# Kernel tuning notes

Hardware: AMD Instinct MI355X
Metric: run time of the kernel (lower is better)

The kernel has to match this reference:

```python
import jax, jax.numpy as jnp
import numpy as np

H = 64  # hidden_dim


def _gru_cell(x, h, W_ih, W_hh, b_ih, b_hh):
    # PyTorch GRU gate order: reset (r), update (z), new (n)
    gx = x @ W_ih.T + b_ih            # [B, 3H]
    gh = h @ W_hh.T + b_hh            # [B, 3H]
    xr, xz, xn = jnp.split(gx, 3, axis=-1)
    hr, hz, hn = jnp.split(gh, 3, axis=-1)
    r = jax.nn.sigmoid(xr + hr)
    z = jax.nn.sigmoid(xz + hz)
    n = jnp.tanh(xn + r * hn)
    return (1.0 - z) * n + z * h


def setup_inputs() -> dict:
    key = jax.random.key(0)
    ks = jax.random.split(key, 11)
    B, T, F_in, A = 1024, 512, 128, 18
    s = 0.05
    return {
        "state": jax.random.normal(ks[0], (B, T, F_in), dtype=jnp.float32),
        "W_ih_l0": jax.random.normal(ks[1], (3 * H, F_in), dtype=jnp.float32) * s,
        "W_hh_l0": jax.random.normal(ks[2], (3 * H, H), dtype=jnp.float32) * s,
        "b_ih_l0": jax.random.normal(ks[3], (3 * H,), dtype=jnp.float32) * s,
        "b_hh_l0": jax.random.normal(ks[4], (3 * H,), dtype=jnp.float32) * s,
        "W_ih_l1": jax.random.normal(ks[5], (3 * H, H), dtype=jnp.float32) * s,
        "W_hh_l1": jax.random.normal(ks[6], (3 * H, H), dtype=jnp.float32) * s,
        "b_ih_l1": jax.random.normal(ks[7], (3 * H,), dtype=jnp.float32) * s,
        "b_hh_l1": jax.random.normal(ks[8], (3 * H,), dtype=jnp.float32) * s,
        "fc3_w": jax.random.normal(ks[9], (A, H), dtype=jnp.float32) * s,
        "fc3_b": jax.random.normal(ks[10], (A,), dtype=jnp.float32) * s,
    }


def reference(state, W_ih_l0, W_hh_l0, b_ih_l0, b_hh_l0,
              W_ih_l1, W_hh_l1, b_ih_l1, b_hh_l1, fc3_w, fc3_b):
    B = state.shape[0]
    h0 = jnp.zeros((B, H), dtype=state.dtype)
    h1 = jnp.zeros((B, H), dtype=state.dtype)
    xs = jnp.swapaxes(state, 0, 1)  # [T, B, F]

    def step(carry, x_t):
        h0, h1 = carry
        h0 = _gru_cell(x_t, h0, W_ih_l0, W_hh_l0, b_ih_l0, b_hh_l0)
        h1 = _gru_cell(h0, h1, W_ih_l1, W_hh_l1, b_ih_l1, b_hh_l1)
        return (h0, h1), None

    (_, h1_last), _ = jax.lax.scan(step, (h0, h1), xs)
    # out[:, -1] of the top GRU layer == final h1; then relu -> linear
    actions = jax.nn.relu(h1_last) @ fc3_w.T + fc3_b
    return actions
```

## Files before the change

### kernel.cpp

```cpp
#include <hip/hip_runtime.h>


#define Tn 512
#define Fn 128
#define Hn 64
#define An 18
#define HS 72

typedef _Float16 half8 __attribute__((ext_vector_type(8)));
typedef float f32x4 __attribute__((ext_vector_type(4)));

#define MFMA(a, b, c) __builtin_amdgcn_mfma_f32_16x16x32_f16((a), (b), (c), 0, 0, 0)

static __device__ __forceinline__ float sigm(float x) {
    return __builtin_amdgcn_rcpf(1.0f + __builtin_amdgcn_exp2f(-1.4426950408889634f * x));
}
static __device__ __forceinline__ float tanh_f(float x) {
    return 2.0f * __builtin_amdgcn_rcpf(1.0f + __builtin_amdgcn_exp2f(-2.8853900817779268f * x)) - 1.0f;
}

__global__ __launch_bounds__(512) void gru_fused(
    const float* __restrict__ state,
    const float* __restrict__ Wih0, const float* __restrict__ Whh0,
    const float* __restrict__ bih0, const float* __restrict__ bhh0,
    const float* __restrict__ Wih1, const float* __restrict__ Whh1,
    const float* __restrict__ bih1, const float* __restrict__ bhh1,
    const float* __restrict__ fcw, const float* __restrict__ fcb,
    float* __restrict__ out)
{
    const int tid  = threadIdx.x;
    const int wv8  = tid >> 6;
    const int lane = tid & 63, c = lane & 15, q = lane >> 4;
    const int wv   = wv8 & 3;
    const int r0   = blockIdx.x * 16;
    const int gc   = wv * 16 + c;
    const int roleB = (wv8 >= 4);

    __shared__ __align__(16) _Float16 h0buf[2][16 * HS];
    __shared__ __align__(16) _Float16 h1buf[2][16 * HS];
    __shared__ float fbuf[16 * 64];

    for (int i = tid; i < 2 * 16 * HS; i += 512) {
        (&h0buf[0][0])[i] = (_Float16)0.0f;
        (&h1buf[0][0])[i] = (_Float16)0.0f;
    }

    half8 W[18];
    f32x4 bias0, bias1, bias2, bias3;
    f32x4 xf32[8];
    half8 xf[4];
    f32x4 hreg = {0.f, 0.f, 0.f, 0.f};
    const float* srow = state + (size_t)(r0 + c) * (Tn * Fn);

    if (!roleB) {
#pragma unroll
        for (int gsel = 0; gsel < 3; ++gsel) {
            const int g = gsel * 64 + gc;
#pragma unroll
            for (int ks = 0; ks < 4; ++ks) {
                const float* p = Wih0 + g * Fn + ks * 32 + q * 8;
#pragma unroll
                for (int j = 0; j < 8; ++j) W[gsel * 4 + ks][j] = (_Float16)p[j];
            }
#pragma unroll
            for (int ks = 0; ks < 2; ++ks) {
                const float* p = Whh0 + g * Hn + ks * 32 + q * 8;
#pragma unroll
                for (int j = 0; j < 8; ++j) W[12 + gsel * 2 + ks][j] = (_Float16)p[j];
            }
        }
        {
            const float b0 = bih0[gc] + bhh0[gc];
            const float b1 = bih0[64 + gc] + bhh0[64 + gc];
            const float b2 = bih0[128 + gc];
            const float b3 = bhh0[128 + gc];
            bias0 = (f32x4){b0, b0, b0, b0};
            bias1 = (f32x4){b1, b1, b1, b1};
            bias2 = (f32x4){b2, b2, b2, b2};
            bias3 = (f32x4){b3, b3, b3, b3};
        }
#pragma unroll
        for (int ks = 0; ks < 4; ++ks) {
            xf32[2 * ks]     = *(const f32x4*)(srow + ks * 32 + q * 8);
            xf32[2 * ks + 1] = *(const f32x4*)(srow + ks * 32 + q * 8 + 4);
        }
#pragma unroll
        for (int ks = 0; ks < 4; ++ks)
#pragma unroll
            for (int i = 0; i < 4; ++i) {
                xf[ks][i]     = (_Float16)xf32[2 * ks][i];
                xf[ks][4 + i] = (_Float16)xf32[2 * ks + 1][i];
            }
#pragma unroll
        for (int ks = 0; ks < 4; ++ks) {
            xf32[2 * ks]     = *(const f32x4*)(srow + Fn + ks * 32 + q * 8);
            xf32[2 * ks + 1] = *(const f32x4*)(srow + Fn + ks * 32 + q * 8 + 4);
        }
    } else {
#pragma unroll
        for (int gsel = 0; gsel < 3; ++gsel) {
            const int g = gsel * 64 + gc;
#pragma unroll
            for (int ks = 0; ks < 2; ++ks) {
                const float* pa = Wih1 + g * Hn + ks * 32 + q * 8;
                const float* pb = Whh1 + g * Hn + ks * 32 + q * 8;
#pragma unroll
                for (int j = 0; j < 8; ++j) {
                    W[gsel * 2 + ks][j]     = (_Float16)pa[j];
                    W[6 + gsel * 2 + ks][j] = (_Float16)pb[j];
                }
            }
        }
        const float br_ = bih1[gc] + bhh1[gc];
        const float bz_ = bih1[64 + gc] + bhh1[64 + gc];
        const float bxn = bih1[128 + gc];
        const float bhn = bhh1[128 + gc];
        bias0 = (f32x4){br_, br_, br_, br_};
        bias1 = (f32x4){bz_, bz_, bz_, bz_};
        bias2 = (f32x4){bxn, bxn, bxn, bxn};
        bias3 = (f32x4){bhn, bhn, bhn, bhn};
    }

    const int ardr = c * HS + q * 8;
    const int wrow = (q * 4) * HS + gc;
    const f32x4 z4 = {0.f, 0.f, 0.f, 0.f};

    for (int t = 0; t <= Tn; ++t) {
        __syncthreads();
        const int pr = (t & 1) ^ 1, pw = t & 1;
        if (!roleB) {
            if (t < Tn) {
                const half8 hf0 = *(const half8*)&h0buf[pr][ardr];
                const half8 hf1 = *(const half8*)&h0buf[pr][ardr + 32];
                __builtin_amdgcn_s_setprio(1);
                f32x4 ar = MFMA(xf[0], W[0], bias0);  ar = MFMA(xf[1], W[1], ar);
                f32x4 az = MFMA(xf[0], W[4], bias1);  az = MFMA(xf[1], W[5], az);
                f32x4 an = MFMA(xf[0], W[8], bias2);  an = MFMA(xf[1], W[9], an);
                f32x4 br = MFMA(xf[2], W[2], z4);     br = MFMA(xf[3], W[3], br);
                f32x4 bz = MFMA(xf[2], W[6], z4);     bz = MFMA(xf[3], W[7], bz);
                f32x4 bn = MFMA(xf[2], W[10], z4);    bn = MFMA(xf[3], W[11], bn);
                br = MFMA(hf0, W[12], br);  br = MFMA(hf1, W[13], br);
                bz = MFMA(hf0, W[14], bz);  bz = MFMA(hf1, W[15], bz);
                f32x4 hn = MFMA(hf0, W[16], bias3);  hn = MFMA(hf1, W[17], hn);
                __builtin_amdgcn_s_setprio(0);
                if (t < Tn - 1) {
#pragma unroll
                    for (int ks = 0; ks < 4; ++ks)
#pragma unroll
                        for (int i = 0; i < 4; ++i) {
                            xf[ks][i]     = (_Float16)xf32[2 * ks][i];
                            xf[ks][4 + i] = (_Float16)xf32[2 * ks + 1][i];
                        }
                    const int tnx = (t + 2 < Tn) ? (t + 2) : (Tn - 1);
#pragma unroll
                    for (int ks = 0; ks < 4; ++ks) {
                        xf32[2 * ks]     = *(const f32x4*)(srow + (size_t)tnx * Fn + ks * 32 + q * 8);
                        xf32[2 * ks + 1] = *(const f32x4*)(srow + (size_t)tnx * Fn + ks * 32 + q * 8 + 4);
                    }
                }
                const f32x4 accr  = ar + br;
                const f32x4 accz  = az + bz;
                const f32x4 accxn = an + bn;
#pragma unroll
                for (int i = 0; i < 4; ++i) {
                    const float rg = sigm(accr[i]);
                    const float zg = sigm(accz[i]);
                    const float ng = tanh_f(accxn[i] + rg * hn[i]);
                    hreg[i] = ng + zg * (hreg[i] - ng);
                }
#pragma unroll
                for (int i = 0; i < 4; ++i) h0buf[pw][wrow + i * HS] = (_Float16)hreg[i];
            }
        } else {
            if (t >= 1) {
                const half8 xf0 = *(const half8*)&h0buf[pr][ardr];
                const half8 xf1 = *(const half8*)&h0buf[pr][ardr + 32];
                const half8 hf0 = *(const half8*)&h1buf[pw][ardr];
                const half8 hf1 = *(const half8*)&h1buf[pw][ardr + 32];
                __builtin_amdgcn_s_setprio(1);
                f32x4 xr = MFMA(xf0, W[0], bias0);  xr = MFMA(xf1, W[1], xr);
                f32x4 xz = MFMA(xf0, W[2], bias1);  xz = MFMA(xf1, W[3], xz);
                f32x4 xn = MFMA(xf0, W[4], bias2);  xn = MFMA(xf1, W[5], xn);
                f32x4 hr = MFMA(hf0, W[6], z4);     hr = MFMA(hf1, W[7], hr);
                f32x4 hz = MFMA(hf0, W[8], z4);     hz = MFMA(hf1, W[9], hz);
                f32x4 hn = MFMA(hf0, W[10], bias3); hn = MFMA(hf1, W[11], hn);
                __builtin_amdgcn_s_setprio(0);
                const f32x4 accr = xr + hr;
                const f32x4 accz = xz + hz;
#pragma unroll
                for (int i = 0; i < 4; ++i) {
                    const float rg = sigm(accr[i]);
                    const float zg = sigm(accz[i]);
                    const float ng = tanh_f(xn[i] + rg * hn[i]);
                    hreg[i] = ng + zg * (hreg[i] - ng);
                }
#pragma unroll
                for (int i = 0; i < 4; ++i) h1buf[pr][wrow + i * HS] = (_Float16)hreg[i];
            }
        }
    }

    if (roleB) {
#pragma unroll
        for (int i = 0; i < 4; ++i) fbuf[(q * 4 + i) * 64 + gc] = fmaxf(hreg[i], 0.0f);
    }
    __syncthreads();
    for (int idx = tid; idx < 16 * An; idx += 512) {
        const int row = idx / An, a = idx - row * An;
        float acc = fcb[a];
#pragma unroll 16
        for (int k = 0; k < Hn; ++k) acc += fbuf[row * 64 + k] * fcw[a * Hn + k];
        out[(size_t)(r0 + row) * An + a] = acc;
    }
}

extern "C" void kernel_launch(void* const* d_in, const int* in_sizes, int n_in,
                              void* d_out, int out_size, void* d_ws, size_t ws_size,
                              hipStream_t stream) {
    const float* state = (const float*)d_in[0];
    const float* Wih0  = (const float*)d_in[1];
    const float* Whh0  = (const float*)d_in[2];
    const float* bih0  = (const float*)d_in[3];
    const float* bhh0  = (const float*)d_in[4];
    const float* Wih1  = (const float*)d_in[5];
    const float* Whh1  = (const float*)d_in[6];
    const float* bih1  = (const float*)d_in[7];
    const float* bhh1  = (const float*)d_in[8];
    const float* fcw   = (const float*)d_in[9];
    const float* fcb   = (const float*)d_in[10];
    float* out = (float*)d_out;

    gru_fused<<<64, 512, 0, stream>>>(state, Wih0, Whh0, bih0, bhh0,
                                      Wih1, Whh1, bih1, bhh1, fcw, fcb, out);
}
```

Baseline: 800.7 us.

## Double-buffer input prefetch three steps ahead and relax per-step barrier

Input rows for layer 0 now go into two alternating f32 register buffers, so loads are issued three timesteps ahead instead of two, giving global loads more time to land before conversion. The per-step __syncthreads is replaced by an LDS-only waitcnt plus a raw s_barrier, so outstanding global prefetches no longer have to drain at each step. The hidden-state MFMA chains are split into separate accumulators to shorten the dependency chain, and launch bounds request two blocks per CU. The extra buffer raises register pressure, which may conflict with the occupancy hint.

```diff
diff --git a/kernel.cpp b/kernel.cpp
--- a/kernel.cpp
+++ b/kernel.cpp
@@ -19,7 +19,26 @@
     return 2.0f * __builtin_amdgcn_rcpf(1.0f + __builtin_amdgcn_exp2f(-2.8853900817779268f * x)) - 1.0f;
 }
 
-__global__ __launch_bounds__(512) void gru_fused(
+#define LOADX(Gbuf, tt) do {                                              \
+    const float* _p = srow + (size_t)(tt) * Fn;                           \
+    _Pragma("unroll")                                                     \
+    for (int _ks = 0; _ks < 4; ++_ks) {                                   \
+        Gbuf[2 * _ks]     = *(const f32x4*)(_p + _ks * 32 + q * 8);       \
+        Gbuf[2 * _ks + 1] = *(const f32x4*)(_p + _ks * 32 + q * 8 + 4);   \
+    }                                                                     \
+} while (0)
+
+#define CVTX(Gbuf) do {                                                   \
+    _Pragma("unroll")                                                     \
+    for (int _ks = 0; _ks < 4; ++_ks)                                     \
+        _Pragma("unroll")                                                 \
+        for (int _i = 0; _i < 4; ++_i) {                                  \
+            xf[_ks][_i]     = (_Float16)Gbuf[2 * _ks][_i];                \
+            xf[_ks][4 + _i] = (_Float16)Gbuf[2 * _ks + 1][_i];            \
+        }                                                                 \
+} while (0)
+
+__global__ __launch_bounds__(512, 2) void gru_fused(
     const float* __restrict__ state,
     const float* __restrict__ Wih0, const float* __restrict__ Whh0,
     const float* __restrict__ bih0, const float* __restrict__ bhh0,
@@ -47,7 +66,7 @@
 
     half8 W[18];
     f32x4 bias0, bias1, bias2, bias3;
-    f32x4 xf32[8];
+    f32x4 GA[8], GB[8];
     half8 xf[4];
     f32x4 hreg = {0.f, 0.f, 0.f, 0.f};
     const float* srow = state + (size_t)(r0 + c) * (Tn * Fn);
@@ -79,23 +98,10 @@
             bias2 = (f32x4){b2, b2, b2, b2};
             bias3 = (f32x4){b3, b3, b3, b3};
         }
-#pragma unroll
-        for (int ks = 0; ks < 4; ++ks) {
-            xf32[2 * ks]     = *(const f32x4*)(srow + ks * 32 + q * 8);
-            xf32[2 * ks + 1] = *(const f32x4*)(srow + ks * 32 + q * 8 + 4);
-        }
-#pragma unroll
-        for (int ks = 0; ks < 4; ++ks)
-#pragma unroll
-            for (int i = 0; i < 4; ++i) {
-                xf[ks][i]     = (_Float16)xf32[2 * ks][i];
-                xf[ks][4 + i] = (_Float16)xf32[2 * ks + 1][i];
-            }
-#pragma unroll
-        for (int ks = 0; ks < 4; ++ks) {
-            xf32[2 * ks]     = *(const f32x4*)(srow + Fn + ks * 32 + q * 8);
-            xf32[2 * ks + 1] = *(const f32x4*)(srow + Fn + ks * 32 + q * 8 + 4);
-        }
+        LOADX(GA, 0);
+        LOADX(GB, 1);
+        CVTX(GA);
+        LOADX(GA, 2);
     } else {
 #pragma unroll
         for (int gsel = 0; gsel < 3; ++gsel) {
@@ -126,7 +132,9 @@
     const f32x4 z4 = {0.f, 0.f, 0.f, 0.f};
 
     for (int t = 0; t <= Tn; ++t) {
-        __syncthreads();
+        asm volatile("s_waitcnt lgkmcnt(0)" ::: "memory");
+        __builtin_amdgcn_s_barrier();
+        asm volatile("" ::: "memory");
         const int pr = (t & 1) ^ 1, pw = t & 1;
         if (!roleB) {
             if (t < Tn) {
@@ -139,27 +147,17 @@
                 f32x4 br = MFMA(xf[2], W[2], z4);     br = MFMA(xf[3], W[3], br);
                 f32x4 bz = MFMA(xf[2], W[6], z4);     bz = MFMA(xf[3], W[7], bz);
                 f32x4 bn = MFMA(xf[2], W[10], z4);    bn = MFMA(xf[3], W[11], bn);
-                br = MFMA(hf0, W[12], br);  br = MFMA(hf1, W[13], br);
-                bz = MFMA(hf0, W[14], bz);  bz = MFMA(hf1, W[15], bz);
-                f32x4 hn = MFMA(hf0, W[16], bias3);  hn = MFMA(hf1, W[17], hn);
+                f32x4 hr = MFMA(hf0, W[12], z4);      hr = MFMA(hf1, W[13], hr);
+                f32x4 hz = MFMA(hf0, W[14], z4);      hz = MFMA(hf1, W[15], hz);
+                f32x4 hn = MFMA(hf0, W[16], bias3);   hn = MFMA(hf1, W[17], hn);
                 __builtin_amdgcn_s_setprio(0);
                 if (t < Tn - 1) {
-#pragma unroll
-                    for (int ks = 0; ks < 4; ++ks)
-#pragma unroll
-                        for (int i = 0; i < 4; ++i) {
-                            xf[ks][i]     = (_Float16)xf32[2 * ks][i];
-                            xf[ks][4 + i] = (_Float16)xf32[2 * ks + 1][i];
-                        }
-                    const int tnx = (t + 2 < Tn) ? (t + 2) : (Tn - 1);
-#pragma unroll
-                    for (int ks = 0; ks < 4; ++ks) {
-                        xf32[2 * ks]     = *(const f32x4*)(srow + (size_t)tnx * Fn + ks * 32 + q * 8);
-                        xf32[2 * ks + 1] = *(const f32x4*)(srow + (size_t)tnx * Fn + ks * 32 + q * 8 + 4);
-                    }
-                }
-                const f32x4 accr  = ar + br;
-                const f32x4 accz  = az + bz;
+                    const int tnx = (t + 3 < Tn) ? (t + 3) : (Tn - 1);
+                    if ((t & 1) == 0) { CVTX(GB); LOADX(GB, tnx); }
+                    else              { CVTX(GA); LOADX(GA, tnx); }
+                }
+                const f32x4 accr  = (ar + br) + hr;
+                const f32x4 accz  = (az + bz) + hz;
                 const f32x4 accxn = an + bn;
 #pragma unroll
                 for (int i = 0; i < 4; ++i) {
```

After: 995.7 us. 1.24x slower.
